# Optimization experiments

Hardware: AMD Instinct MI355X
Metric: run time of the kernel (lower is better)

The kernel has to match this reference:

```python
import jax, jax.numpy as jnp
import numpy as np

B, S, D, H = 1, 4096, 1024, 16
HD = D // H  # head_dim = 64
NEG = -1e9

def setup_inputs() -> dict:
    key = jax.random.key(0)
    ks = jax.random.split(key, 5)
    scale = 1.0 / np.sqrt(D)
    x = jax.random.normal(ks[0], (B, S, D), dtype=jnp.float32)
    Wq = jax.random.normal(ks[1], (D, D), dtype=jnp.float32) * scale
    Wk = jax.random.normal(ks[2], (D, D), dtype=jnp.float32) * scale
    Wv = jax.random.normal(ks[3], (D, D), dtype=jnp.float32) * scale
    Wo = jax.random.normal(ks[4], (D, D), dtype=jnp.float32) * scale
    mask = jnp.tril(jnp.ones((S, S), dtype=bool))[None, None]  # [1,1,S,S] causal
    return {"x": x, "mask": mask, "Wq": Wq, "Wk": Wk, "Wv": Wv, "Wo": Wo}

def reference(x, mask, Wq, Wk, Wv, Wo):
    # Linear projections (bias=False). nn.Linear computes x @ W.T; weights here
    # are stored as [out, in] so we use x @ W.T for faithfulness.
    q = x @ Wq.T  # [B,S,D]
    k = x @ Wk.T
    v = x @ Wv.T
    def split_heads(t):
        return t.reshape(B, S, H, HD).transpose(0, 2, 1, 3)  # [B,H,S,HD]
    q, k, v = split_heads(q), split_heads(k), split_heads(v)
    scores = jnp.einsum("bhqd,bhkd->bhqk", q, k) / jnp.sqrt(jnp.float32(HD))
    scores = jnp.where(mask, scores, NEG)
    attn = jax.nn.softmax(scores, axis=-1)  # dropout p=0.0 -> identity
    out = jnp.einsum("bhqk,bhkd->bhqd", attn, v)  # [B,H,S,HD]
    out = out.transpose(0, 2, 1, 3).reshape(B, S, D)
    return out @ Wo.T
```

## Files before the change

kernel.cpp:

```cpp
#include <hip/hip_runtime.h>
#include <hip/hip_bf16.h>


typedef __bf16 bf16x8 __attribute__((ext_vector_type(8)));
typedef __bf16 bf16x4 __attribute__((ext_vector_type(4)));
typedef float f32x4 __attribute__((ext_vector_type(4)));
typedef short s16x4 __attribute__((ext_vector_type(4)));

#define GAS __attribute__((address_space(1)))
#define LAS __attribute__((address_space(3)))

__device__ __forceinline__ void async_copy16(const void* g, void* l) {
  __builtin_amdgcn_global_load_lds((const GAS unsigned int*)g,
                                   (LAS unsigned int*)l, 16, 0, 0);
}

__device__ __forceinline__ f32x4 mfma_k16(bf16x4 a, bf16x4 b, f32x4 c) {
  union { bf16x4 h; s16x4 s; } ua, ub;
  ua.h = a; ub.h = b;
  return __builtin_amdgcn_mfma_f32_16x16x16bf16_1k(ua.s, ub.s, c, 0, 0, 0);
}

__global__ __launch_bounds__(256) void cvt_all(const float* __restrict__ x,
                                               const float* __restrict__ Wq,
                                               const float* __restrict__ Wk,
                                               const float* __restrict__ Wv,
                                               const float* __restrict__ Wo,
                                               __bf16* __restrict__ xb,
                                               __bf16* __restrict__ Wc,
                                               __bf16* __restrict__ Wob) {
  int b = blockIdx.x;
  const float* src;
  __bf16* dst;
  if (b < 4096)      { src = x  + (b       ) * 1024; dst = xb  + (long)b * 1024; }
  else if (b < 5120) { src = Wq + (b - 4096) * 1024; dst = Wc  + (long)(b - 4096) * 1024; }
  else if (b < 6144) { src = Wk + (b - 5120) * 1024; dst = Wc  + (1l << 20) + (long)(b - 5120) * 1024; }
  else if (b < 7168) { src = Wv + (b - 6144) * 1024; dst = Wc  + (2l << 20) + (long)(b - 6144) * 1024; }
  else               { src = Wo + (b - 7168) * 1024; dst = Wob + (long)(b - 7168) * 1024; }
  int i = threadIdx.x * 4;
  float4 f = *(const float4*)(src + i);
  bf16x4 o;
  o[0] = (__bf16)f.x; o[1] = (__bf16)f.y; o[2] = (__bf16)f.z; o[3] = (__bf16)f.w;
  *(bf16x4*)(dst + i) = o;
}

__global__ __launch_bounds__(256) void gemm_qkv(const __bf16* __restrict__ A,
                                                const __bf16* __restrict__ B,
                                                __bf16* __restrict__ Qb,
                                                __bf16* __restrict__ Kf,
                                                __bf16* __restrict__ Vf) {
  const int K = 1024;
  __shared__ __bf16 As[128 * 32];
  __shared__ __bf16 Bs[128 * 32];
  const int tid = threadIdx.x;
  const int lane = tid & 63, wv = tid >> 6;
  const int l15 = lane & 15, quad = lane >> 4;
  const int wm = wv >> 1, wn = wv & 1;
  const int mbase = blockIdx.y * 128, nbase = blockIdx.x * 128;
  const bool kswap = (nbase >= 1024) && (nbase < 2048);

  f32x4 acc[4][4] = {};

  for (int k0 = 0; k0 < K; k0 += 32) {
    __syncthreads();
#pragma unroll
    for (int q = 0; q < 2; ++q) {
      int i = q * 256 + tid;
      int row = i >> 2, kg = i & 3;
      const __bf16* ga = A + (long)(mbase + row) * K + k0 + kg * 8;
      const __bf16* gb = B + (long)(nbase + row) * K + k0 + kg * 8;
      char* la = (char*)As + (q * 256 + wv * 64) * 16;
      char* lb = (char*)Bs + (q * 256 + wv * 64) * 16;
      async_copy16(ga, la);
      async_copy16(gb, lb);
    }
    __syncthreads();
    bf16x8 af[4], bfr[4];
#pragma unroll
    for (int i = 0; i < 4; ++i)
      af[i] = *(const bf16x8*)&As[(wm * 64 + i * 16 + l15) * 32 + quad * 8];
#pragma unroll
    for (int j = 0; j < 4; ++j)
      bfr[j] = *(const bf16x8*)&Bs[(wn * 64 + j * 16 + l15) * 32 + quad * 8];
    if (kswap) {
#pragma unroll
      for (int i = 0; i < 4; ++i)
#pragma unroll
        for (int j = 0; j < 4; ++j)
          acc[i][j] = __builtin_amdgcn_mfma_f32_16x16x32_bf16(bfr[j], af[i], acc[i][j], 0, 0, 0);
    } else {
#pragma unroll
      for (int i = 0; i < 4; ++i)
#pragma unroll
        for (int j = 0; j < 4; ++j)
          acc[i][j] = __builtin_amdgcn_mfma_f32_16x16x32_bf16(af[i], bfr[j], acc[i][j], 0, 0, 0);
    }
  }

  if (nbase < 1024) {
    const float QS = 0.18033688011112043f;
#pragma unroll
    for (int i = 0; i < 4; ++i)
#pragma unroll
      for (int j = 0; j < 4; ++j) {
        int col = nbase + wn * 64 + j * 16 + l15;
#pragma unroll
        for (int r = 0; r < 4; ++r) {
          int row = mbase + wm * 64 + i * 16 + quad * 4 + r;
          Qb[(long)row * 1024 + col] = (__bf16)(acc[i][j][r] * QS);
        }
      }
  } else if (nbase < 2048) {
#pragma unroll
    for (int i = 0; i < 4; ++i)
#pragma unroll
      for (int j = 0; j < 4; ++j) {
        int d0 = nbase - 1024 + wn * 64 + j * 16 + quad * 4;
        int h = d0 >> 6, dd = d0 & 63;
        int kk = dd >> 5, qf = (dd >> 3) & 3, e0 = dd & 7;
        int kt = mbase + wm * 64 + i * 16 + l15;
        int tile = kt >> 6;
        long off = ((long)(h * 64 + tile) * 8 + i * 2 + kk) * 512 + (qf * 16 + l15) * 8 + e0;
        union { __bf16 b[4]; uint2 u; } pk;
#pragma unroll
        for (int r = 0; r < 4; ++r) pk.b[r] = (__bf16)acc[i][j][r];
        *(uint2*)(Kf + off) = pk.u;
      }
  } else {
#pragma unroll
    for (int i = 0; i < 4; ++i)
#pragma unroll
      for (int j = 0; j < 4; ++j) {
        int col = nbase - 2048 + wn * 64 + j * 16 + l15;
        int h = col >> 6, dd = col & 63;
        int jd = dd >> 4, lv = dd & 15;
        int kt0 = mbase + wm * 64 + i * 16 + quad * 4;
        int tile = kt0 >> 6, w6 = kt0 & 63;
        int jp = w6 >> 5, bit4 = (w6 >> 4) & 1, qv = (w6 >> 2) & 3;
        long off = ((long)(h * 64 + tile) * 8 + jd * 2 + jp) * 512 + (qv * 16 + lv) * 8 + bit4 * 4;
        union { __bf16 b[4]; uint2 u; } pk;
#pragma unroll
        for (int r = 0; r < 4; ++r) pk.b[r] = (__bf16)acc[i][j][r];
        *(uint2*)(Vf + off) = pk.u;
      }
  }
}

__global__ __launch_bounds__(256) void gemm_wo(const __bf16* __restrict__ A,
                                               const __bf16* __restrict__ B,
                                               float* __restrict__ C) {
  const int K = 1024, N = 1024;
  __shared__ __bf16 As[128 * 32];
  __shared__ __bf16 Bs[128 * 32];
  const int tid = threadIdx.x;
  const int lane = tid & 63, wv = tid >> 6;
  const int l15 = lane & 15, quad = lane >> 4;
  const int wm = wv >> 1, wn = wv & 1;
  const int mbase = blockIdx.y * 128, nbase = blockIdx.x * 128;

  f32x4 acc[4][4] = {};

  for (int k0 = 0; k0 < K; k0 += 32) {
    __syncthreads();
#pragma unroll
    for (int q = 0; q < 2; ++q) {
      int i = q * 256 + tid;
      int row = i >> 2, kg = i & 3;
      const __bf16* ga = A + (long)(mbase + row) * K + k0 + kg * 8;
      const __bf16* gb = B + (long)(nbase + row) * K + k0 + kg * 8;
      char* la = (char*)As + (q * 256 + wv * 64) * 16;
      char* lb = (char*)Bs + (q * 256 + wv * 64) * 16;
      async_copy16(ga, la);
      async_copy16(gb, lb);
    }
    __syncthreads();
    bf16x8 af[4], bfr[4];
#pragma unroll
    for (int i = 0; i < 4; ++i)
      af[i] = *(const bf16x8*)&As[(wm * 64 + i * 16 + l15) * 32 + quad * 8];
#pragma unroll
    for (int j = 0; j < 4; ++j)
      bfr[j] = *(const bf16x8*)&Bs[(wn * 64 + j * 16 + l15) * 32 + quad * 8];
#pragma unroll
    for (int i = 0; i < 4; ++i)
#pragma unroll
      for (int j = 0; j < 4; ++j)
        acc[i][j] = __builtin_amdgcn_mfma_f32_16x16x32_bf16(af[i], bfr[j], acc[i][j], 0, 0, 0);
  }
#pragma unroll
  for (int i = 0; i < 4; ++i)
#pragma unroll
    for (int j = 0; j < 4; ++j)
#pragma unroll
      for (int r = 0; r < 4; ++r) {
        int row = mbase + wm * 64 + i * 16 + quad * 4 + r;
        int col = nbase + wn * 64 + j * 16 + l15;
        C[(long)row * N + col] = acc[i][j][r];
      }
}

__global__ __launch_bounds__(512, 4) void flash_attn(const __bf16* __restrict__ Qb,
                                                     const __bf16* __restrict__ Kf,
                                                     const __bf16* __restrict__ Vf,
                                                     __bf16* __restrict__ AO) {
  __shared__ float Ms[4][64][17];
  const int tid = threadIdx.x;
  const int lane = tid & 63, l15 = lane & 15, quad = lane >> 4;
  const int w = tid >> 6;
  const int pr = w >> 1, half = w & 1;
  const int b = blockIdx.x;
  const int h = (b & 7) + 8 * ((b >> 3) & 1);
  const int g = b >> 4;
  const int p = g * 4 + pr;
  const int hoff = h * 64;

  const __bf16* Kh = Kf + (long)h * 64 * 4096;
  const __bf16* Vh = Vf + (long)h * 64 * 4096;

#pragma unroll
  for (int pass = 0; pass < 2; ++pass) {
    const int t = pass ? (255 - p) : p;
    const int qrow = t * 16 + l15;
    bf16x8 qf[2];
    qf[0] = *(const bf16x8*)(Qb + (long)qrow * 1024 + hoff + quad * 8);
    qf[1] = *(const bf16x8*)(Qb + (long)qrow * 1024 + hoff + 32 + quad * 8);

    const int nkt = (t >> 2) + 1;
    const int kt0 = half ? (nkt >> 1) : 0;
    const int kt1 = half ? nkt : (nkt >> 1);
    f32x4 o_acc[4] = {};
    float l_acc = 0.0f;

    bf16x8 kc[8];
    if (kt0 < kt1) {
      const __bf16* Kt = Kh + (long)kt0 * 4096;
#pragma unroll
      for (int f = 0; f < 8; ++f)
        kc[f] = *(const bf16x8*)(Kt + f * 512 + lane * 8);
    }

    for (int kt = kt0; kt < kt1; ++kt) {
      const __bf16* Vt = Vh + (long)kt * 4096;

      bf16x8 va[8];
#pragma unroll
      for (int f = 0; f < 8; ++f)
        va[f] = *(const bf16x8*)(Vt + f * 512 + lane * 8);

      f32x4 st[4] = {};
#pragma unroll
      for (int j = 0; j < 4; ++j) {
        st[j] = __builtin_amdgcn_mfma_f32_16x16x32_bf16(kc[j * 2 + 0], qf[0], st[j], 0, 0, 0);
        st[j] = __builtin_amdgcn_mfma_f32_16x16x32_bf16(kc[j * 2 + 1], qf[1], st[j], 0, 0, 0);
      }

      if (kt + 1 < kt1) {
        const __bf16* Kt = Kh + (long)(kt + 1) * 4096;
#pragma unroll
        for (int f = 0; f < 8; ++f)
          kc[f] = *(const bf16x8*)(Kt + f * 512 + lane * 8);
      }

      if (kt == nkt - 1) {
        const int dq = (t & 3) * 16 + l15;
#pragma unroll
        for (int j = 0; j < 4; ++j)
#pragma unroll
          for (int r = 0; r < 4; ++r)
            if (j * 16 + quad * 4 + r > dq) st[j][r] = -3.0e38f;
      }

      bf16x4 pb[4];
      float ps = 0.0f;
#pragma unroll
      for (int j = 0; j < 4; ++j) {
        f32x4 pj;
#pragma unroll
        for (int r = 0; r < 4; ++r) pj[r] = __builtin_amdgcn_exp2f(st[j][r]);
        ps += (pj[0] + pj[1]) + (pj[2] + pj[3]);
        bf16x4 bb;
#pragma unroll
        for (int r = 0; r < 4; ++r) bb[r] = (__bf16)pj[r];
        pb[j] = bb;
      }
      l_acc += ps;

#pragma unroll
      for (int j = 0; j < 4; ++j) {
        bf16x4 pbj = pb[j];
#pragma unroll
        for (int jd = 0; jd < 4; ++jd) {
          bf16x8 v8 = va[jd * 2 + (j >> 1)];
          bf16x4 a4 = (j & 1) ? __builtin_shufflevector(v8, v8, 4, 5, 6, 7)
                              : __builtin_shufflevector(v8, v8, 0, 1, 2, 3);
          o_acc[jd] = mfma_k16(a4, pbj, o_acc[jd]);
        }
      }
    }

    if (half) {
#pragma unroll
      for (int jd = 0; jd < 4; ++jd)
#pragma unroll
        for (int r = 0; r < 4; ++r)
          Ms[pr][lane][jd * 4 + r] = o_acc[jd][r];
      Ms[pr][lane][16] = l_acc;
    }
    __syncthreads();
    if (!half) {
#pragma unroll
      for (int jd = 0; jd < 4; ++jd)
#pragma unroll
        for (int r = 0; r < 4; ++r)
          o_acc[jd][r] += Ms[pr][lane][jd * 4 + r];
      l_acc += Ms[pr][lane][16];

      l_acc += __shfl_xor(l_acc, 16);
      l_acc += __shfl_xor(l_acc, 32);
      const float inv = 1.0f / l_acc;

#pragma unroll
      for (int jd = 0; jd < 4; ++jd) {
        bf16x4 ob;
#pragma unroll
        for (int r = 0; r < 4; ++r) ob[r] = (__bf16)(o_acc[jd][r] * inv);
        *(bf16x4*)(AO + (long)qrow * 1024 + hoff + jd * 16 + quad * 4) = ob;
      }
    }
    __syncthreads();
  }
}

extern "C" void kernel_launch(void* const* d_in, const int* in_sizes, int n_in,
                              void* d_out, int out_size, void* d_ws, size_t ws_size,
                              hipStream_t stream) {
  const float* x  = (const float*)d_in[0];
  const float* Wq = (const float*)d_in[2];
  const float* Wk = (const float*)d_in[3];
  const float* Wv = (const float*)d_in[4];
  const float* Wo = (const float*)d_in[5];
  float* out = (float*)d_out;

  char* ws = (char*)d_ws;
  __bf16* xb  = (__bf16*)ws;
  __bf16* Wc  = (__bf16*)(ws + (8u << 20));
  __bf16* Wob = (__bf16*)(ws + (14u << 20));
  __bf16* Qb  = (__bf16*)(ws + (16u << 20));
  __bf16* Kfr = (__bf16*)(ws + (24u << 20));
  __bf16* Vfr = (__bf16*)(ws + (32u << 20));
  __bf16* AO  = (__bf16*)(ws + (40u << 20));

  cvt_all<<<8192, 256, 0, stream>>>(x, Wq, Wk, Wv, Wo, xb, Wc, Wob);

  dim3 g1(3072 / 128, 4096 / 128);
  gemm_qkv<<<g1, 256, 0, stream>>>(xb, Wc, Qb, Kfr, Vfr);

  flash_attn<<<512, 512, 0, stream>>>(Qb, Kfr, Vfr, AO);

  dim3 g2(1024 / 128, 4096 / 128);
  gemm_wo<<<g2, 256, 0, stream>>>(AO, Wob, out);
}
```

Before: 257.9 us.

## Process two query tiles per warp in flash attention; narrow Wo GEMM tiles

Each flash-attention warp now handles 32 query rows as two 16-row groups that share the same K and V fragments per key tile, which halves global K/V loads per query and halves the grid to 256 blocks. Launch bounds drop to 2 blocks per SM to make room for the doubled accumulator registers. The output-projection GEMM moves to 128x64 tiles, doubling its block count so more CUs are busy on the small N=1024 problem. The risks are lower occupancy and parallelism in attention, and less operand reuse per block in the GEMM.

```diff
diff --git a/kernel.cpp b/kernel.cpp
--- a/kernel.cpp
+++ b/kernel.cpp
@@ -151,14 +151,14 @@
                                                float* __restrict__ C) {
   const int K = 1024, N = 1024;
   __shared__ __bf16 As[128 * 32];
-  __shared__ __bf16 Bs[128 * 32];
+  __shared__ __bf16 Bs[64 * 32];
   const int tid = threadIdx.x;
   const int lane = tid & 63, wv = tid >> 6;
   const int l15 = lane & 15, quad = lane >> 4;
   const int wm = wv >> 1, wn = wv & 1;
-  const int mbase = blockIdx.y * 128, nbase = blockIdx.x * 128;
-
-  f32x4 acc[4][4] = {};
+  const int mbase = blockIdx.y * 128, nbase = blockIdx.x * 64;
+
+  f32x4 acc[4][2] = {};
 
   for (int k0 = 0; k0 < K; k0 += 32) {
     __syncthreads();
@@ -167,69 +167,74 @@
       int i = q * 256 + tid;
       int row = i >> 2, kg = i & 3;
       const __bf16* ga = A + (long)(mbase + row) * K + k0 + kg * 8;
+      char* la = (char*)As + (q * 256 + wv * 64) * 16;
+      async_copy16(ga, la);
+    }
+    {
+      int row = tid >> 2, kg = tid & 3;
       const __bf16* gb = B + (long)(nbase + row) * K + k0 + kg * 8;
-      char* la = (char*)As + (q * 256 + wv * 64) * 16;
-      char* lb = (char*)Bs + (q * 256 + wv * 64) * 16;
-      async_copy16(ga, la);
+      char* lb = (char*)Bs + (wv * 64) * 16;
       async_copy16(gb, lb);
     }
     __syncthreads();
-    bf16x8 af[4], bfr[4];
+    bf16x8 af[4], bfr[2];
 #pragma unroll
     for (int i = 0; i < 4; ++i)
       af[i] = *(const bf16x8*)&As[(wm * 64 + i * 16 + l15) * 32 + quad * 8];
 #pragma unroll
-    for (int j = 0; j < 4; ++j)
-      bfr[j] = *(const bf16x8*)&Bs[(wn * 64 + j * 16 + l15) * 32 + quad * 8];
-#pragma unroll
-    for (int i = 0; i < 4; ++i)
-#pragma unroll
-      for (int j = 0; j < 4; ++j)
+    for (int j = 0; j < 2; ++j)
+      bfr[j] = *(const bf16x8*)&Bs[(wn * 32 + j * 16 + l15) * 32 + quad * 8];
+#pragma unroll
+    for (int i = 0; i < 4; ++i)
+#pragma unroll
+      for (int j = 0; j < 2; ++j)
         acc[i][j] = __builtin_amdgcn_mfma_f32_16x16x32_bf16(af[i], bfr[j], acc[i][j], 0, 0, 0);
   }
 #pragma unroll
   for (int i = 0; i < 4; ++i)
 #pragma unroll
-    for (int j = 0; j < 4; ++j)
+    for (int j = 0; j < 2; ++j)
 #pragma unroll
       for (int r = 0; r < 4; ++r) {
         int row = mbase + wm * 64 + i * 16 + quad * 4 + r;
-        int col = nbase + wn * 64 + j * 16 + l15;
+        int col = nbase + wn * 32 + j * 16 + l15;
         C[(long)row * N + col] = acc[i][j][r];
       }
 }
 
-__global__ __launch_bounds__(512, 4) void flash_attn(const __bf16* __restrict__ Qb,
+__global__ __launch_bounds__(512, 2) void flash_attn(const __bf16* __restrict__ Qb,
                                                      const __bf16* __restrict__ Kf,
                                                      const __bf16* __restrict__ Vf,
                                                      __bf16* __restrict__ AO) {
-  __shared__ float Ms[4][64][17];
+  __shared__ float Ms[4][64][35];
   const int tid = threadIdx.x;
   const int lane = tid & 63, l15 = lane & 15, quad = lane >> 4;
   const int w = tid >> 6;
   const int pr = w >> 1, half = w & 1;
   const int b = blockIdx.x;
   const int h = (b & 7) + 8 * ((b >> 3) & 1);
-  const int g = b >> 4;
-  const int p = g * 4 + pr;
+  const int rest = b >> 4;
+  const int P = rest * 4 + pr;
   const int hoff = h * 64;
 
   const __bf16* Kh = Kf + (long)h * 64 * 4096;
   const __bf16* Vh = Vf + (long)h * 64 * 4096;
 
-#pragma unroll
   for (int pass = 0; pass < 2; ++pass) {
-    const int t = pass ? (255 - p) : p;
-    const int qrow = t * 16 + l15;
-    bf16x8 qf[2];
-    qf[0] = *(const bf16x8*)(Qb + (long)qrow * 1024 + hoff + quad * 8);
-    qf[1] = *(const bf16x8*)(Qb + (long)qrow * 1024 + hoff + 32 + quad * 8);
-
-    const int nkt = (t >> 2) + 1;
+    const int T = pass ? (127 - P) : P;
+    bf16x8 qf[2][2];
+#pragma unroll
+    for (int g = 0; g < 2; ++g) {
+      const int qrow = T * 32 + g * 16 + l15;
+      qf[g][0] = *(const bf16x8*)(Qb + (long)qrow * 1024 + hoff + quad * 8);
+      qf[g][1] = *(const bf16x8*)(Qb + (long)qrow * 1024 + hoff + 32 + quad * 8);
+    }
+
+    const int nkt = (T >> 1) + 1;
     const int kt0 = half ? (nkt >> 1) : 0;
     const int kt1 = half ? nkt : (nkt >> 1);
-    f32x4 o_acc[4] = {};
-    float l_acc = 0.0f;
+    f32x4 o_acc[2][4] = {};
+    float l_acc[2] = {0.0f, 0.0f};
 
     bf16x8 kc[8];
     if (kt0 < kt1) {
@@ -247,12 +252,14 @@
       for (int f = 0; f < 8; ++f)
         va[f] = *(const bf16x8*)(Vt + f * 512 + lane * 8);
 
-      f32x4 st[4] = {};
-#pragma unroll
-      for (int j = 0; j < 4; ++j) {
-        st[j] = __builtin_amdgcn_mfma_f32_16x16x32_bf16(kc[j * 2 + 0], qf[0], st[j], 0, 0, 0);
-        st[j] = __builtin_amdgcn_mfma_f32_16x16x32_bf16(kc[j * 2 + 1], qf[1], st[j], 0, 0, 0);
-      }
+      f32x4 st[2][4] = {};
+#pragma unroll
+      for (int g = 0; g < 2; ++g)
+#pragma unroll
+        for (int j = 0; j < 4; ++j) {
+          st[g][j] = __builtin_amdgcn_mfma_f32_16x16x32_bf16(kc[j * 2 + 0], qf[g][0], st[g][j], 0, 0, 0);
+          st[g][j] = __builtin_amdgcn_mfma_f32_16x16x32_bf16(kc[j * 2 + 1], qf[g][1], st[g][j], 0, 0, 0);
+        }
 
       if (kt + 1 < kt1) {
         const __bf16* Kt = Kh + (long)(kt + 1) * 4096;
@@ -262,69 +269,82 @@
       }
 
       if (kt == nkt - 1) {
-        const int dq = (t & 3) * 16 + l15;
-#pragma unroll
-        for (int j = 0; j < 4; ++j)
+#pragma unroll
+        for (int g = 0; g < 2; ++g) {
+          const int dq = (T & 1) * 32 + g * 16 + l15;
+#pragma unroll
+          for (int j = 0; j < 4; ++j)
+#pragma unroll
+            for (int r = 0; r < 4; ++r)
+              if (j * 16 + quad * 4 + r > dq) st[g][j][r] = -3.0e38f;
+        }
+      }
+
+      bf16x4 pb[2][4];
+#pragma unroll
+      for (int g = 0; g < 2; ++g) {
+        float ps = 0.0f;
+#pragma unroll
+        for (int j = 0; j < 4; ++j) {
+          f32x4 pj;
+#pragma unroll
+          for (int r = 0; r < 4; ++r) pj[r] = __builtin_amdgcn_exp2f(st[g][j][r]);
+          ps += (pj[0] + pj[1]) + (pj[2] + pj[3]);
+          bf16x4 bb;
+#pragma unroll
+          for (int r = 0; r < 4; ++r) bb[r] = (__bf16)pj[r];
+          pb[g][j] = bb;
+        }
+        l_acc[g] += ps;
+      }
+
+#pragma unroll
+      for (int g = 0; g < 2; ++g)
+#pragma unroll
+        for (int j = 0; j < 4; ++j) {
+          bf16x4 pbj = pb[g][j];
+#pragma unroll
+          for (int jd = 0; jd < 4; ++jd) {
+            bf16x8 v8 = va[jd * 2 + (j >> 1)];
+            bf16x4 a4 = (j & 1) ? __builtin_shufflevector(v8, v8, 4, 5, 6, 7)
+                                : __builtin_shufflevector(v8, v8, 0, 1, 2, 3);
+            o_acc[g][jd] = mfma_k16(a4, pbj, o_acc[g][jd]);
+          }
+        }
+    }
+
+    if (half) {
+#pragma unroll
+      for (int g = 0; g < 2; ++g) {
+#pragma unroll
+        for (int jd = 0; jd < 4; ++jd)
 #pragma unroll
           for (int r = 0; r < 4; ++r)
-            if (j * 16 + quad * 4 + r > dq) st[j][r] = -3.0e38f;
-      }
-
-      bf16x4 pb[4];
-      float ps = 0.0f;
-#pragma unroll
-      for (int j = 0; j < 4; ++j) {
-        f32x4 pj;
-#pragma unroll
-        for (int r = 0; r < 4; ++r) pj[r] = __builtin_amdgcn_exp2f(st[j][r]);
-        ps += (pj[0] + pj[1]) + (pj[2] + pj[3]);
-        bf16x4 bb;
-#pragma unroll
-        for (int r = 0; r < 4; ++r) bb[r] = (__bf16)pj[r];
-        pb[j] = bb;
-      }
-      l_acc += ps;
-
-#pragma unroll
-      for (int j = 0; j < 4; ++j) {
-        bf16x4 pbj = pb[j];
+            Ms[pr][lane][g * 16 + jd * 4 + r] = o_acc[g][jd][r];
+        Ms[pr][lane][32 + g] = l_acc[g];
+      }
+    }
+    __syncthreads();
+    if (!half) {
+#pragma unroll
+      for (int g = 0; g < 2; ++g) {
+#pragma unroll
+        for (int jd = 0; jd < 4; ++jd)
+#pragma unroll
+          for (int r = 0; r < 4; ++r)
+            o_acc[g][jd][r] += Ms[pr][lane][g * 16 + jd * 4 + r];
+        float la = l_acc[g] + Ms[pr][lane][32 + g];
+        la += __shfl_xor(la, 16);
+        la += __shfl_xor(la, 32);
+        const float inv = 1.0f / la;
+        const int qrow = T * 32 + g * 16 + l15;
 #pragma unroll
         for (int jd = 0; jd < 4; ++jd) {
-          bf16x8 v8 = va[jd * 2 + (j >> 1)];
-          bf16x4 a4 = (j & 1) ? __builtin_shufflevector(v8, v8, 4, 5, 6, 7)
-                              : __builtin_shufflevector(v8, v8, 0, 1, 2, 3);
-          o_acc[jd] = mfma_k16(a4, pbj, o_acc[jd]);
-        }
-      }
-    }
-
-    if (half) {
-#pragma unroll
-      for (int jd = 0; jd < 4; ++jd)
-#pragma unroll
-        for (int r = 0; r < 4; ++r)
-          Ms[pr][lane][jd * 4 + r] = o_acc[jd][r];
-      Ms[pr][lane][16] = l_acc;
-    }
-    __syncthreads();
-    if (!half) {
-#pragma unroll
-      for (int jd = 0; jd < 4; ++jd)
-#pragma unroll
-        for (int r = 0; r < 4; ++r)
-          o_acc[jd][r] += Ms[pr][lane][jd * 4 + r];
-      l_acc += Ms[pr][lane][16];
-
-      l_acc += __shfl_xor(l_acc, 16);
-      l_acc += __shfl_xor(l_acc, 32);
-      const float inv = 1.0f / l_acc;
-
-#pragma unroll
-      for (int jd = 0; jd < 4; ++jd) {
-        bf16x4 ob;
-#pragma unroll
-        for (int r = 0; r < 4; ++r) ob[r] = (__bf16)(o_acc[jd][r] * inv);
-        *(bf16x4*)(AO + (long)qrow * 1024 + hoff + jd * 16 + quad * 4) = ob;
+          bf16x4 ob;
+#pragma unroll
+          for (int r = 0; r < 4; ++r) ob[r] = (__bf16)(o_acc[g][jd][r] * inv);
+          *(bf16x4*)(AO + (long)qrow * 1024 + hoff + jd * 16 + quad * 4) = ob;
+        }
       }
     }
     __syncthreads();
@@ -355,8 +375,8 @@
   dim3 g1(3072 / 128, 4096 / 128);
   gemm_qkv<<<g1, 256, 0, stream>>>(xb, Wc, Qb, Kfr, Vfr);
 
-  flash_attn<<<512, 512, 0, stream>>>(Qb, Kfr, Vfr, AO);
-
-  dim3 g2(1024 / 128, 4096 / 128);
+  flash_attn<<<256, 512, 0, stream>>>(Qb, Kfr, Vfr, AO);
+
+  dim3 g2(1024 / 64, 4096 / 128);
   gemm_wo<<<g2, 256, 0, stream>>>(AO, Wob, out);
 }
```

After: 232.4 us. -9.9%, faster.
